# Kernel optimization log

Measured on AMD Instinct MI355X. Metric: run time of the kernel, lower is better.

## Reference

```python
import jax, jax.numpy as jnp
import numpy as np

EPS = 1e-6
N_HEADS, N_POINTS = 6, 4


def layer_norm(x, w, b):
    m = jnp.mean(x, -1, keepdims=True)
    v = jnp.mean((x - m) ** 2, -1, keepdims=True)
    return (x - m) * jax.lax.rsqrt(v + EPS) * w + b


def bilinear_sample(val, loc, Hl, Wl):
    # val: (B, nH, Hl*Wl, d); loc: (B, Lq, nH, P, 2) in [0,1]
    # matches F.grid_sample(mode='bilinear', padding='zeros', align_corners=False)
    B, nH, _, d = val.shape
    Lq, P = loc.shape[1], loc.shape[3]
    x = loc[..., 0] * Wl - 0.5
    y = loc[..., 1] * Hl - 0.5
    x0 = jnp.floor(x)
    y0 = jnp.floor(y)
    wx1 = x - x0
    wy1 = y - y0
    out = jnp.zeros((B, nH, Lq * P, d), val.dtype)
    corners = ((0, 0, (1 - wy1) * (1 - wx1)), (0, 1, (1 - wy1) * wx1),
               (1, 0, wy1 * (1 - wx1)), (1, 1, wy1 * wx1))
    for dy, dx, w in corners:
        xi = x0 + dx
        yi = y0 + dy
        valid = (xi >= 0) & (xi < Wl) & (yi >= 0) & (yi < Hl)
        xi_c = jnp.clip(xi, 0, Wl - 1).astype(jnp.int32)
        yi_c = jnp.clip(yi, 0, Hl - 1).astype(jnp.int32)
        idx = (yi_c * Wl + xi_c).transpose(0, 2, 1, 3).reshape(B, nH, Lq * P)
        g = jnp.take_along_axis(val, idx[..., None], axis=2)  # (B,nH,Lq*P,d)
        ww = jnp.where(valid, w, 0.0).transpose(0, 2, 1, 3).reshape(B, nH, Lq * P)
        out = out + g * ww[..., None]
    return out.reshape(B, nH, Lq, P, d).transpose(0, 2, 1, 3, 4)  # (B,Lq,nH,P,d)


def dwconv3x3(x, w, b):
    # x: (N, C, H, W); w: (C, 1, 3, 3) depthwise
    y = jax.lax.conv_general_dilated(x, w, (1, 1), 'SAME',
                                     feature_group_count=w.shape[0],
                                     dimension_numbers=('NCHW', 'OIHW', 'NCHW'))
    return y + b[None, :, None, None]


def setup_inputs() -> dict:
    key = jax.random.key(0)
    ks = jax.random.split(key, 16)
    B, H, W, C = 8, 32, 32, 768
    Lq = 3 * H * W
    Hf = Wf = 64
    hidden = int(C * 0.25)
    s = 0.02
    inp = {
        'query': jax.random.normal(ks[0], (B, Lq, C), jnp.float32),
        'reference_points': jax.random.uniform(ks[1], (B, Lq, 1, 2), jnp.float32),
        'feat': jax.random.normal(ks[2], (B, Hf * Wf, C), jnp.float32),
        'spatial_shapes': jnp.array([[Hf, Wf]], jnp.int32),
        'level_start_index': jnp.zeros((1,), jnp.int32),
        'H': H, 'W': W,
        'qn_w': jnp.ones((C,)), 'qn_b': jnp.zeros((C,)),
        'fn_w': jnp.ones((C,)), 'fn_b': jnp.zeros((C,)),
        'so_w': jax.random.normal(ks[3], (C, N_HEADS * N_POINTS * 2)) * s,
        'so_b': jax.random.normal(ks[4], (N_HEADS * N_POINTS * 2,)) * s,
        'aw_w': jax.random.normal(ks[5], (C, N_HEADS * N_POINTS)) * s,
        'aw_b': jnp.zeros((N_HEADS * N_POINTS,)),
        'vp_w': jax.random.normal(ks[6], (C, C)) * s,
        'vp_b': jnp.zeros((C,)),
        'op_w': jax.random.normal(ks[7], (C, C)) * s,
        'op_b': jnp.zeros((C,)),
        'ffn_w': jnp.ones((C,)), 'ffn_b': jnp.zeros((C,)),
        'fc1_w': jax.random.normal(ks[8], (C, hidden)) * s,
        'fc1_b': jnp.zeros((hidden,)),
        'dw_w': jax.random.normal(ks[9], (hidden, 1, 3, 3)) * s,
        'dw_b': jnp.zeros((hidden,)),
        'fc2_w': jax.random.normal(ks[10], (hidden, C)) * s,
        'fc2_b': jnp.zeros((C,)),
    }
    return inp


def reference(query, reference_points, feat, spatial_shapes, level_start_index, H, W,
              qn_w, qn_b, fn_w, fn_b, so_w, so_b, aw_w, aw_b, vp_w, vp_b, op_w, op_b,
              ffn_w, ffn_b, fc1_w, fc1_b, dw_w, dw_b, fc2_w, fc2_b):
    B, Lq, C = query.shape
    nH, nP = N_HEADS, N_POINTS
    d = C // nH
    ss = np.asarray(spatial_shapes)
    Hl, Wl = int(ss[0, 0]), int(ss[0, 1])

    # --- MSDeformAttn (single level) ---
    q = layer_norm(query, qn_w, qn_b)
    f = layer_norm(feat, fn_w, fn_b)
    value = (f @ vp_w + vp_b).reshape(B, Hl * Wl, nH, d).transpose(0, 2, 1, 3)  # (B,nH,Lin,d)
    offs = (q @ so_w + so_b).reshape(B, Lq, nH, 1, nP, 2)
    aw = jax.nn.softmax((q @ aw_w + aw_b).reshape(B, Lq, nH, nP), axis=-1)
    normalizer = jnp.array([Wl, Hl], query.dtype)
    loc = reference_points[:, :, None, :, None, :] + offs / normalizer  # (B,Lq,nH,1,nP,2)
    sampled = bilinear_sample(value, loc[:, :, :, 0], Hl, Wl)           # (B,Lq,nH,nP,d)
    attn = (sampled * aw[..., None]).sum(3).reshape(B, Lq, C) @ op_w + op_b
    query = query + attn

    # --- ConvFFN (3 equal HxW chunks through shared depthwise conv) ---
    x = layer_norm(query, ffn_w, ffn_b) @ fc1_w + fc1_b  # (B, 3*H*W, hid)
    n = Lq // 3
    hid = fc1_w.shape[1]
    xc = x.reshape(B, 3, n, hid).transpose(0, 1, 3, 2).reshape(B * 3, hid, H, W)
    xc = dwconv3x3(xc, dw_w, dw_b)
    x = xc.reshape(B, 3, hid, n).transpose(0, 1, 3, 2).reshape(B, Lq, hid)
    x = jax.nn.gelu(x, approximate=False)
    x = x @ fc2_w + fc2_b
    return query + x
```

## Files before the change

### kernel.cpp

```cpp
#include <hip/hip_runtime.h>
#include <hip/hip_bf16.h>
#include <math.h>

typedef __hip_bfloat16 bf16;
typedef short bf16x8 __attribute__((ext_vector_type(8)));
typedef short bf16x4 __attribute__((ext_vector_type(4)));
typedef float f32x4 __attribute__((ext_vector_type(4)));

#define NB 8
#define LQ 3072
#define CC 768
#define NHEADS 6
#define NPTS 4
#define DHEAD 128
#define HLVL 64
#define WLVL 64
#define LIN 4096
#define HID 192
#define BLTOT 24576
#define FROWS 32768

__device__ __forceinline__ float bf2f(short u)
{ return __uint_as_float(((unsigned)(unsigned short)u) << 16); }

template<int N_>
__device__ __forceinline__ void wait_vmcnt()
{
    if constexpr (N_ == 0)      asm volatile("s_waitcnt vmcnt(0)" ::: "memory");
    else if constexpr (N_ == 2) asm volatile("s_waitcnt vmcnt(2)" ::: "memory");
    else if constexpr (N_ == 4) asm volatile("s_waitcnt vmcnt(4)" ::: "memory");
    else if constexpr (N_ == 6) asm volatile("s_waitcnt vmcnt(6)" ::: "memory");
    else if constexpr (N_ == 8) asm volatile("s_waitcnt vmcnt(8)" ::: "memory");
    else static_assert(N_ == 0, "add a vmcnt case");
}

__device__ __forceinline__ void wt_tile(float (*t)[65], const float* __restrict__ src,
                                        bf16* __restrict__ dst, int K, int N, int tn0, int tk0)
{
    const int r = threadIdx.x >> 6, c = threadIdx.x & 63;
    #pragma unroll
    for (int i = 0; i < 16; ++i)
        t[i * 4 + r][c] = src[(size_t)(tk0 + i * 4 + r) * N + tn0 + c];
    __syncthreads();
    #pragma unroll
    for (int i = 0; i < 16; ++i)
        dst[(size_t)(tn0 + i * 4 + r) * K + tk0 + c] = __float2bfloat16(t[c][i * 4 + r]);
}

__global__ __launch_bounds__(256)
void prep_kernel(const float* __restrict__ vp_w, const float* __restrict__ op_w,
                 const float* __restrict__ fc1_w, const float* __restrict__ fc2_w,
                 const float* __restrict__ so_w, const float* __restrict__ so_b,
                 const float* __restrict__ aw_w, const float* __restrict__ aw_b,
                 const float* __restrict__ feat, const float* __restrict__ fn_w,
                 const float* __restrict__ fn_b,
                 bf16* __restrict__ vp_wt, bf16* __restrict__ op_wt,
                 bf16* __restrict__ fc1_wt, bf16* __restrict__ fc2_wt,
                 bf16* __restrict__ dots_wt, float* __restrict__ db,
                 bf16* __restrict__ f_ln)
{
    __shared__ float t[64][65];
    int b = blockIdx.x;
    if (b < 144)      wt_tile(t, vp_w, vp_wt, 768, 768, (b % 12) * 64, (b / 12) * 64);
    else if (b < 288) { b -= 144; wt_tile(t, op_w, op_wt, 768, 768, (b % 12) * 64, (b / 12) * 64); }
    else if (b < 324) { b -= 288; wt_tile(t, fc1_w, fc1_wt, 768, 192, (b % 3) * 64, (b / 3) * 64); }
    else if (b < 360) { b -= 324; wt_tile(t, fc2_w, fc2_wt, 192, 768, (b % 12) * 64, (b / 12) * 64); }
    else if (b < 744) {
        b -= 360;
        int i = b * 256 + threadIdx.x;
        if (i < 128 * 768) {
            int n = i / 768, k = i - n * 768;
            float v = 0.f;
            if (n < 48) v = so_w[(size_t)k * 48 + n];
            else if (n < 72) v = aw_w[(size_t)k * 24 + (n - 48)];
            dots_wt[i] = __float2bfloat16(v);
        }
        if (i < 128) {
            float bv = 0.f;
            if (i < 48) bv = so_b[i];
            else if (i < 72) bv = aw_b[i - 48];
            db[i] = bv;
        }
    } else {
        const int row = (b - 744) * 4 + (threadIdx.x >> 6);
        const int lane = threadIdx.x & 63;
        const f32x4* xr = (const f32x4*)(feat + (size_t)row * CC);
        f32x4 f0 = xr[lane], f1 = xr[64 + lane], f2 = xr[128 + lane];
        float s = 0.f, ss = 0.f;
        #pragma unroll
        for (int k = 0; k < 4; ++k) {
            s += f0[k] + f1[k] + f2[k];
            ss += f0[k] * f0[k] + f1[k] * f1[k] + f2[k] * f2[k];
        }
        #pragma unroll
        for (int o = 32; o > 0; o >>= 1) { s += __shfl_down(s, o); ss += __shfl_down(ss, o); }
        s = __shfl(s, 0); ss = __shfl(ss, 0);
        const float m = s * (1.f / CC);
        const float rs = rsqrtf(ss * (1.f / CC) - m * m + 1e-6f);
        const f32x4* w4 = (const f32x4*)fn_w;
        const f32x4* b4 = (const f32x4*)fn_b;
        bf16* orow = f_ln + (size_t)row * CC;
        #pragma unroll
        for (int j = 0; j < 3; ++j) {
            f32x4 fj = (j == 0) ? f0 : (j == 1) ? f1 : f2;
            f32x4 wj = w4[j * 64 + lane], bj = b4[j * 64 + lane];
            bf16 t4[4];
            #pragma unroll
            for (int k = 0; k < 4; ++k) t4[k] = __float2bfloat16((fj[k] - m) * rs * wj[k] + bj[k]);
            *(bf16x4*)(orow + j * 256 + lane * 4) = *(bf16x4*)t4;
        }
    }
}

template<int BM, int BN, int WM, int WN, int MODE>
__global__ __launch_bounds__(256)
void gemm_kernel(const bf16* __restrict__ A, const bf16* __restrict__ Bt,
                 const float* __restrict__ bias, const void* __restrict__ resv,
                 void* __restrict__ outv, int M, int N, int K)
{
    constexpr int WAVES_N = BN / WN;
    constexpr int FM = WM / 16, FN = WN / 16;
    constexpr int CWA = BM / 32;
    constexpr int CWB = BN / 32;
    constexpr int LPT = CWA + CWB;
    constexpr int ABYTES = BM * 256;
    constexpr int DBUF_BYTES = (BM + BN) * 256;
    constexpr int EPI_BYTES = BM * BN * 4;
    constexpr size_t SMEM_BYTES = DBUF_BYTES > EPI_BYTES ? DBUF_BYTES : EPI_BYTES;
    __shared__ __align__(16) char smem[SMEM_BYTES];
    bf16* sA = (bf16*)smem;
    bf16* sB = (bf16*)(smem + ABYTES);
    float* epi = (float*)smem;

    const int tid = threadIdx.x;
    const int lane = tid & 63;
    const int wave = tid >> 6;

    const int nwgx = gridDim.x;
    const int nwg = nwgx * gridDim.y;
    const int bid = blockIdx.y * nwgx + blockIdx.x;
    const int swz = (bid & 7) * (nwg >> 3) + (bid >> 3);
    const int m0 = (swz / nwgx) * BM;
    const int n0 = (swz % nwgx) * BN;

    const int wm = (wave / WAVES_N) * WM;
    const int wn = (wave % WAVES_N) * WN;

    const int srow = lane >> 3;
    const int scol = ((lane & 7) ^ srow) * 8;

    constexpr int GPR8 = BN / 8;
    constexpr int GPT8 = (BM * BN / 8) / 256;
    constexpr int QPR4 = BN / 4;
    constexpr int QPT4 = (BM * BN / 4) / 256;
    float4 pr0[GPT8], pr1[GPT8];
    bf16x4 prb[QPT4];
    if constexpr (MODE == 3) {
        const float* resf = (const float*)resv;
        #pragma unroll
        for (int k = 0; k < GPT8; ++k) {
            const int f = k * 256 + tid;
            const int rr = f / GPR8, cc = (f % GPR8) * 8;
            const size_t gidx = (size_t)(m0 + rr) * N + n0 + cc;
            pr0[k] = *(const float4*)&resf[gidx];
            pr1[k] = *(const float4*)&resf[gidx + 4];
        }
    }
    if constexpr (MODE == 4) {
        const bf16* resb = (const bf16*)resv;
        #pragma unroll
        for (int k = 0; k < QPT4; ++k) {
            const int f = k * 256 + tid;
            const int rr = f / QPR4, cc = (f % QPR4) * 4;
            prb[k] = *(const bf16x4*)&resb[(size_t)(m0 + rr) * N + n0 + cc];
        }
    }

#define STAGE(tt, half)                                                                            \
    { const int k0_ = (tt) * 64;                                                                   \
      _Pragma("unroll")                                                                            \
      for (int i_ = 0; i_ < CWA; ++i_) {                                                           \
        const int c_ = i_ * 4 + wave;                                                              \
        __builtin_amdgcn_global_load_lds(                                                          \
          (const __attribute__((address_space(1))) void*)(A + (size_t)(m0 + c_ * 8 + srow) * K + k0_ + scol), \
          (__attribute__((address_space(3))) void*)(sA + (half) * (BM * 64) + c_ * 512), 16, 0, 0); } \
      _Pragma("unroll")                                                                            \
      for (int i_ = 0; i_ < CWB; ++i_) {                                                           \
        const int c_ = i_ * 4 + wave;                                                              \
        __builtin_amdgcn_global_load_lds(                                                          \
          (const __attribute__((address_space(1))) void*)(Bt + (size_t)(n0 + c_ * 8 + srow) * K + k0_ + scol), \
          (__attribute__((address_space(3))) void*)(sB + (half) * (BN * 64) + c_ * 512), 16, 0, 0); } }

    f32x4 acc[FM][FN] = {};
    const int nt = K >> 6;

    STAGE(0, 0);
    STAGE(1, 1);

    for (int t = 0; t < nt; ++t) {
        const int half = t & 1;
        if (t + 1 < nt) wait_vmcnt<LPT>();
        else            wait_vmcnt<0>();
        __builtin_amdgcn_s_barrier();
        const bf16* cA = sA + half * (BM * 64);
        const bf16* cB = sB + half * (BN * 64);
        #pragma unroll
        for (int kki = 0; kki < 2; ++kki) {
            const int kslot = kki * 4 + (lane >> 4);
            bf16x8 aF[FM], bF[FN];
            #pragma unroll
            for (int i = 0; i < FM; ++i) {
                const int row = wm + i * 16 + (lane & 15);
                aF[i] = *(const bf16x8*)(&cA[row * 64 + ((kslot ^ (row & 7)) * 8)]);
            }
            #pragma unroll
            for (int j = 0; j < FN; ++j) {
                const int row = wn + j * 16 + (lane & 15);
                bF[j] = *(const bf16x8*)(&cB[row * 64 + ((kslot ^ (row & 7)) * 8)]);
            }
            #pragma unroll
            for (int i = 0; i < FM; ++i) {
                #pragma unroll
                for (int j = 0; j < FN; ++j)
                    acc[i][j] = __builtin_amdgcn_mfma_f32_16x16x32_bf16(aF[i], bF[j], acc[i][j], 0, 0, 0);
            }
        }
        asm volatile("s_waitcnt lgkmcnt(0)" ::: "memory");
        __builtin_amdgcn_s_barrier();
        if (t + 2 < nt) STAGE(t + 2, half);
    }
#undef STAGE

    #pragma unroll
    for (int j = 0; j < FN; ++j) {
        const int colL = wn + j * 16 + (lane & 15);
        const float bj = bias[n0 + colL];
        #pragma unroll
        for (int i = 0; i < FM; ++i) {
            #pragma unroll
            for (int r = 0; r < 4; ++r) {
                const int rowL = wm + i * 16 + ((lane >> 4) << 2) + r;
                const int addr = rowL * BN + ((((colL >> 2) ^ (rowL & 7)) << 2) | (colL & 3));
                epi[addr] = acc[i][j][r] + bj;
            }
        }
    }
    __syncthreads();

    if constexpr (MODE == 0 || MODE == 3) {
        #pragma unroll
        for (int k = 0; k < GPT8; ++k) {
            const int f = k * 256 + tid;
            const int rr = f / GPR8, cc = (f % GPR8) * 8;
            const int g0 = ((cc >> 2) ^ (rr & 7)) << 2;
            const int g1 = (((cc >> 2) + 1) ^ (rr & 7)) << 2;
            float4 v0 = *(const float4*)&epi[rr * BN + g0];
            float4 v1 = *(const float4*)&epi[rr * BN + g1];
            if constexpr (MODE == 3) {
                v0.x += pr0[k].x; v0.y += pr0[k].y; v0.z += pr0[k].z; v0.w += pr0[k].w;
                v1.x += pr1[k].x; v1.y += pr1[k].y; v1.z += pr1[k].z; v1.w += pr1[k].w;
            }
            bf16 tmp[8];
            tmp[0] = __float2bfloat16(v0.x); tmp[1] = __float2bfloat16(v0.y);
            tmp[2] = __float2bfloat16(v0.z); tmp[3] = __float2bfloat16(v0.w);
            tmp[4] = __float2bfloat16(v1.x); tmp[5] = __float2bfloat16(v1.y);
            tmp[6] = __float2bfloat16(v1.z); tmp[7] = __float2bfloat16(v1.w);
            *(bf16x8*)((bf16*)outv + (size_t)(m0 + rr) * N + n0 + cc) = *(bf16x8*)tmp;
        }
    } else {
        #pragma unroll
        for (int k = 0; k < QPT4; ++k) {
            const int f = k * 256 + tid;
            const int rr = f / QPR4, cc = (f % QPR4) * 4;
            const int gs = ((cc >> 2) ^ (rr & 7)) << 2;
            float4 v = *(const float4*)&epi[rr * BN + gs];
            if constexpr (MODE == 4) {
                v.x += bf2f(prb[k][0]); v.y += bf2f(prb[k][1]);
                v.z += bf2f(prb[k][2]); v.w += bf2f(prb[k][3]);
            }
            *(float4*)&((float*)outv)[(size_t)(m0 + rr) * N + n0 + cc] = v;
        }
    }
}

__global__ __launch_bounds__(512)
void gemm_value_kernel(const bf16* __restrict__ A, const bf16* __restrict__ Bt,
                       const float* __restrict__ bias, bf16* __restrict__ outb,
                       int M, int N, int K)
{
    constexpr int BM = 128, BN = 256;
    constexpr int FM = 4, FN = 4;
    constexpr int CWA = 2, CWB = 4;
    constexpr int LPT = CWA + CWB;
    __shared__ __align__(16) char smem[2 * (BM + BN) * 128];
    bf16* sA = (bf16*)smem;
    bf16* sB = (bf16*)(smem + 2 * BM * 128);
    float* epi = (float*)smem;

    const int tid = threadIdx.x;
    const int lane = tid & 63;
    const int wave = tid >> 6;

    const int nwgx = gridDim.x;
    const int nwg = nwgx * gridDim.y;
    const int bid = blockIdx.y * nwgx + blockIdx.x;
    const int swz = (bid & 7) * (nwg >> 3) + (bid >> 3);
    const int m0 = (swz / nwgx) * BM;
    const int n0 = (swz % nwgx) * BN;

    const int wm = (wave >> 2) * 64;
    const int wn = (wave & 3) * 64;
    const int srow = lane >> 3;
    const int scol = ((lane & 7) ^ srow) * 8;

#define STAGEV(tt, half)                                                                           \
    { const int k0_ = (tt) * 64;                                                                   \
      _Pragma("unroll")                                                                            \
      for (int i_ = 0; i_ < CWA; ++i_) {                                                           \
        const int c_ = i_ * 8 + wave;                                                              \
        __builtin_amdgcn_global_load_lds(                                                          \
          (const __attribute__((address_space(1))) void*)(A + (size_t)(m0 + c_ * 8 + srow) * K + k0_ + scol), \
          (__attribute__((address_space(3))) void*)(sA + (half) * (BM * 64) + c_ * 512), 16, 0, 0); } \
      _Pragma("unroll")                                                                            \
      for (int i_ = 0; i_ < CWB; ++i_) {                                                           \
        const int c_ = i_ * 8 + wave;                                                              \
        __builtin_amdgcn_global_load_lds(                                                          \
          (const __attribute__((address_space(1))) void*)(Bt + (size_t)(n0 + c_ * 8 + srow) * K + k0_ + scol), \
          (__attribute__((address_space(3))) void*)(sB + (half) * (BN * 64) + c_ * 512), 16, 0, 0); } }

    f32x4 acc[FM][FN] = {};
    const int nt = K >> 6;

    STAGEV(0, 0);
    STAGEV(1, 1);

    for (int t = 0; t < nt; ++t) {
        const int half = t & 1;
        if (t + 1 < nt) wait_vmcnt<LPT>();
        else            wait_vmcnt<0>();
        __builtin_amdgcn_s_barrier();
        const bf16* cA = sA + half * (BM * 64);
        const bf16* cB = sB + half * (BN * 64);
        #pragma unroll
        for (int kki = 0; kki < 2; ++kki) {
            const int kslot = kki * 4 + (lane >> 4);
            bf16x8 aF[FM], bF[FN];
            #pragma unroll
            for (int i = 0; i < FM; ++i) {
                const int row = wm + i * 16 + (lane & 15);
                aF[i] = *(const bf16x8*)(&cA[row * 64 + ((kslot ^ (row & 7)) * 8)]);
            }
            #pragma unroll
            for (int j = 0; j < FN; ++j) {
                const int row = wn + j * 16 + (lane & 15);
                bF[j] = *(const bf16x8*)(&cB[row * 64 + ((kslot ^ (row & 7)) * 8)]);
            }
            #pragma unroll
            for (int i = 0; i < FM; ++i) {
                #pragma unroll
                for (int j = 0; j < FN; ++j)
                    acc[i][j] = __builtin_amdgcn_mfma_f32_16x16x32_bf16(aF[i], bF[j], acc[i][j], 0, 0, 0);
            }
        }
        asm volatile("s_waitcnt lgkmcnt(0)" ::: "memory");
        __builtin_amdgcn_s_barrier();
        if (t + 2 < nt) STAGEV(t + 2, half);
    }
#undef STAGEV

    for (int half = 0; half < 2; ++half) {
        if ((wave >> 2) == half) {
            #pragma unroll
            for (int j = 0; j < FN; ++j) {
                const int colL = wn + j * 16 + (lane & 15);
                const float bj = bias[n0 + colL];
                #pragma unroll
                for (int i = 0; i < FM; ++i) {
                    #pragma unroll
                    for (int r = 0; r < 4; ++r) {
                        const int lr = i * 16 + ((lane >> 4) << 2) + r;
                        const int addr = lr * BN + ((((colL >> 2) ^ (lr & 7)) << 2) | (colL & 3));
                        epi[addr] = acc[i][j][r] + bj;
                    }
                }
            }
        }
        __syncthreads();
        #pragma unroll
        for (int k = 0; k < 4; ++k) {
            const int f = k * 512 + tid;
            const int rr = f >> 5, cc = (f & 31) * 8;
            const int g0 = ((cc >> 2) ^ (rr & 7)) << 2;
            const int g1 = (((cc >> 2) + 1) ^ (rr & 7)) << 2;
            float4 v0 = *(const float4*)&epi[rr * BN + g0];
            float4 v1 = *(const float4*)&epi[rr * BN + g1];
            bf16 tmp[8];
            tmp[0] = __float2bfloat16(v0.x); tmp[1] = __float2bfloat16(v0.y);
            tmp[2] = __float2bfloat16(v0.z); tmp[3] = __float2bfloat16(v0.w);
            tmp[4] = __float2bfloat16(v1.x); tmp[5] = __float2bfloat16(v1.y);
            tmp[6] = __float2bfloat16(v1.z); tmp[7] = __float2bfloat16(v1.w);
            *(bf16x8*)(outb + (size_t)(m0 + half * 64 + rr) * N + n0 + cc) = *(bf16x8*)tmp;
        }
        __syncthreads();
    }
}

template<int BM, int BN, int WM, int WN, bool F32IN, int EPI>
__global__ __launch_bounds__(256)
void ln_gemm_kernel(const void* __restrict__ xv, const float* __restrict__ lnw,
                    const float* __restrict__ lnb, const bf16* __restrict__ Bt,
                    const float* __restrict__ bias, const float* __restrict__ refp,
                    void* __restrict__ outv, int M, int N)
{
    constexpr int WAVES_N = BN / WN;
    constexpr int FM = WM / 16, FN = WN / 16;
    constexpr int CWB = BN / 32;
    constexpr int RPW = BM / 4;
    static_assert(BM * BN * 4 <= 2 * BN * 64 * 2, "epi must fit in sB");
    __shared__ __align__(16) bf16 sA[BM * 768];
    __shared__ __align__(16) char sBmem[2 * BN * 64 * 2];
    bf16* sB = (bf16*)sBmem;
    float* epi = (float*)sBmem;

    const int tid = threadIdx.x;
    const int lane = tid & 63;
    const int wave = tid >> 6;

    const int nwgx = gridDim.x;
    const int nwg = nwgx * gridDim.y;
    const int bid = blockIdx.y * nwgx + blockIdx.x;
    const int swz = (bid & 7) * (nwg >> 3) + (bid >> 3);
    const int m0 = (swz / nwgx) * BM;
    const int n0 = (swz % nwgx) * BN;

    const int wm = (wave / WAVES_N) * WM;
    const int wn = (wave % WAVES_N) * WN;
    const int srow = lane >> 3;
    const int scol = ((lane & 7) ^ srow) * 8;

#define STAGEB(tt, half)                                                                           \
    { const int k0_ = (tt) * 64;                                                                   \
      _Pragma("unroll")                                                                            \
      for (int i_ = 0; i_ < CWB; ++i_) {                                                           \
        const int c_ = i_ * 4 + wave;                                                              \
        __builtin_amdgcn_global_load_lds(                                                          \
          (const __attribute__((address_space(1))) void*)(Bt + (size_t)(n0 + c_ * 8 + srow) * 768 + k0_ + scol), \
          (__attribute__((address_space(3))) void*)(sB + (half) * (BN * 64) + c_ * 512), 16, 0, 0); } }

    STAGEB(0, 0);
    STAGEB(1, 1);

    if constexpr (F32IN) {
        const f32x4* w4 = (const f32x4*)lnw;
        const f32x4* b4 = (const f32x4*)lnb;
        f32x4 wv0 = w4[lane], wv1 = w4[64 + lane], wv2 = w4[128 + lane];
        f32x4 bv0 = b4[lane], bv1 = b4[64 + lane], bv2 = b4[128 + lane];
        for (int rr = 0; rr < RPW; ++rr) {
            const int r = wave * RPW + rr;
            const f32x4* xr = (const f32x4*)((const float*)xv + (size_t)(m0 + r) * 768);
            f32x4 f0 = xr[lane], f1 = xr[64 + lane], f2 = xr[128 + lane];
            float s = 0.f, ss = 0.f;
            #pragma unroll
            for (int k = 0; k < 4; ++k) {
                s += f0[k] + f1[k] + f2[k];
                ss += f0[k] * f0[k] + f1[k] * f1[k] + f2[k] * f2[k];
            }
            #pragma unroll
            for (int o = 32; o > 0; o >>= 1) { s += __shfl_down(s, o); ss += __shfl_down(ss, o); }
            s = __shfl(s, 0); ss = __shfl(ss, 0);
            const float mn = s * (1.f / 768);
            const float rs = rsqrtf(ss * (1.f / 768) - mn * mn + 1e-6f);
            const int rx7 = r & 7;
            const int slot = (lane >> 1) & 7;
            const int off = (lane & 1) * 4;
            #pragma unroll
            for (int j = 0; j < 3; ++j) {
                f32x4 fj = (j == 0) ? f0 : (j == 1) ? f1 : f2;
                f32x4 wj = (j == 0) ? wv0 : (j == 1) ? wv1 : wv2;
                f32x4 bj = (j == 0) ? bv0 : (j == 1) ? bv1 : bv2;
                bf16 t4[4];
                #pragma unroll
                for (int k = 0; k < 4; ++k)
                    t4[k] = __float2bfloat16((fj[k] - mn) * rs * wj[k] + bj[k]);
                const int kt = j * 4 + (lane >> 4);
                *(bf16x4*)&sA[r * 768 + kt * 64 + ((slot ^ rx7) << 3) + off] = *(bf16x4*)t4;
            }
        }
    } else {
        const f32x4* w4 = (const f32x4*)lnw;
        const f32x4* b4 = (const f32x4*)lnb;
        f32x4 w80 = w4[lane * 2], w81 = w4[lane * 2 + 1], w44 = w4[128 + lane];
        f32x4 b80 = b4[lane * 2], b81 = b4[lane * 2 + 1], b44 = b4[128 + lane];
        for (int rr = 0; rr < RPW; ++rr) {
            const int r = wave * RPW + rr;
            const bf16* xr = (const bf16*)xv + (size_t)(m0 + r) * 768;
            bf16x8 v8 = *(const bf16x8*)(xr + lane * 8);
            bf16x4 v4 = *(const bf16x4*)(xr + 512 + lane * 4);
            float f[12];
            #pragma unroll
            for (int k = 0; k < 8; ++k) f[k] = bf2f(v8[k]);
            #pragma unroll
            for (int k = 0; k < 4; ++k) f[8 + k] = bf2f(v4[k]);
            float s = 0.f, ss = 0.f;
            #pragma unroll
            for (int k = 0; k < 12; ++k) { s += f[k]; ss += f[k] * f[k]; }
            #pragma unroll
            for (int o = 32; o > 0; o >>= 1) { s += __shfl_down(s, o); ss += __shfl_down(ss, o); }
            s = __shfl(s, 0); ss = __shfl(ss, 0);
            const float mn = s * (1.f / 768);
            const float rs = rsqrtf(ss * (1.f / 768) - mn * mn + 1e-6f);
            const int rx7 = r & 7;
            bf16 t8[8];
            #pragma unroll
            for (int k = 0; k < 4; ++k) t8[k] = __float2bfloat16((f[k] - mn) * rs * w80[k] + b80[k]);
            #pragma unroll
            for (int k = 0; k < 4; ++k) t8[4 + k] = __float2bfloat16((f[4 + k] - mn) * rs * w81[k] + b81[k]);
            *(bf16x8*)&sA[r * 768 + (lane >> 3) * 64 + (((lane & 7) ^ rx7) << 3)] = *(bf16x8*)t8;
            bf16 t4[4];
            #pragma unroll
            for (int k = 0; k < 4; ++k) t4[k] = __float2bfloat16((f[8 + k] - mn) * rs * w44[k] + b44[k]);
            *(bf16x4*)&sA[r * 768 + (8 + (lane >> 4)) * 64 + ((((lane >> 1) & 7) ^ rx7) << 3) + (lane & 1) * 4]
                = *(bf16x4*)t4;
        }
    }
    asm volatile("s_waitcnt lgkmcnt(0)" ::: "memory");

    f32x4 acc[FM][FN] = {};
    #pragma unroll
    for (int t = 0; t < 12; ++t) {
        const int half = t & 1;
        if (t + 1 < 12) wait_vmcnt<CWB>();
        else            wait_vmcnt<0>();
        __builtin_amdgcn_s_barrier();
        const bf16* cB = sB + half * (BN * 64);
        #pragma unroll
        for (int kki = 0; kki < 2; ++kki) {
            const int kslot = kki * 4 + (lane >> 4);
            bf16x8 aF[FM], bF[FN];
            #pragma unroll
            for (int i = 0; i < FM; ++i) {
                const int row = wm + i * 16 + (lane & 15);
                aF[i] = *(const bf16x8*)(&sA[row * 768 + t * 64 + ((kslot ^ (row & 7)) * 8)]);
            }
            #pragma unroll
            for (int j = 0; j < FN; ++j) {
                const int row = wn + j * 16 + (lane & 15);
                bF[j] = *(const bf16x8*)(&cB[row * 64 + ((kslot ^ (row & 7)) * 8)]);
            }
            #pragma unroll
            for (int i = 0; i < FM; ++i) {
                #pragma unroll
                for (int j = 0; j < FN; ++j)
                    acc[i][j] = __builtin_amdgcn_mfma_f32_16x16x32_bf16(aF[i], bF[j], acc[i][j], 0, 0, 0);
            }
        }
        asm volatile("s_waitcnt lgkmcnt(0)" ::: "memory");
        __builtin_amdgcn_s_barrier();
        if (t + 2 < 12) STAGEB(t + 2, half);
    }
#undef STAGEB

    #pragma unroll
    for (int j = 0; j < FN; ++j) {
        const int colL = wn + j * 16 + (lane & 15);
        const float bj = bias[n0 + colL];
        #pragma unroll
        for (int i = 0; i < FM; ++i) {
            #pragma unroll
            for (int r = 0; r < 4; ++r) {
                const int rowL = wm + i * 16 + ((lane >> 4) << 2) + r;
                const int addr = rowL * BN + ((((colL >> 2) ^ (rowL & 7)) << 2) | (colL & 3));
                epi[addr] = acc[i][j][r] + bj;
            }
        }
    }
    __syncthreads();

    if constexpr (EPI == 1) {
        if (tid < BM * NHEADS) {
            const int rowL = tid & (BM - 1);
            const int h = tid / BM;
            auto erd = [&](int col) -> float {
                return epi[rowL * BN + ((((col >> 2) ^ (rowL & 7)) << 2) | (col & 3))];
            };
            float l0 = erd(48 + h * 4 + 0), l1 = erd(48 + h * 4 + 1);
            float l2 = erd(48 + h * 4 + 2), l3 = erd(48 + h * 4 + 3);
            float mx = fmaxf(fmaxf(l0, l1), fmaxf(l2, l3));
            float e0 = expf(l0 - mx), e1 = expf(l1 - mx), e2 = expf(l2 - mx), e3 = expf(l3 - mx);
            float inv = 1.f / (e0 + e1 + e2 + e3);
            float ee[4] = {e0, e1, e2, e3};
            const float rx = refp[(size_t)(m0 + rowL) * 2];
            const float ry = refp[(size_t)(m0 + rowL) * 2 + 1];
            float4* pp = (float4*)outv + ((size_t)(m0 + rowL) * NHEADS + h) * 4;
            #pragma unroll
            for (int p = 0; p < 4; ++p) {
                float ox = erd(h * 8 + p * 2), oy = erd(h * 8 + p * 2 + 1);
                pp[p] = make_float4(rx + ox * (1.f / WLVL), ry + oy * (1.f / HLVL), ee[p] * inv, 0.f);
            }
        }
    } else {
        constexpr int GPR8 = BN / 8;
        constexpr int GPT8 = (BM * BN / 8) / 256;
        #pragma unroll
        for (int k = 0; k < GPT8; ++k) {
            const int f = k * 256 + tid;
            const int rr = f / GPR8, cc = (f % GPR8) * 8;
            const int g0 = ((cc >> 2) ^ (rr & 7)) << 2;
            const int g1 = (((cc >> 2) + 1) ^ (rr & 7)) << 2;
            float4 v0 = *(const float4*)&epi[rr * BN + g0];
            float4 v1 = *(const float4*)&epi[rr * BN + g1];
            bf16 tmp[8];
            tmp[0] = __float2bfloat16(v0.x); tmp[1] = __float2bfloat16(v0.y);
            tmp[2] = __float2bfloat16(v0.z); tmp[3] = __float2bfloat16(v0.w);
            tmp[4] = __float2bfloat16(v1.x); tmp[5] = __float2bfloat16(v1.y);
            tmp[6] = __float2bfloat16(v1.z); tmp[7] = __float2bfloat16(v1.w);
            *(bf16x8*)((bf16*)outv + (size_t)(m0 + rr) * N + n0 + cc) = *(bf16x8*)tmp;
        }
    }
}

__global__ __launch_bounds__(256)
void sampler_kernel(const bf16* __restrict__ value, const float4* __restrict__ params,
                    bf16* __restrict__ attn_in)
{
    const int tid = threadIdx.x;
    const int cpx = gridDim.x >> 3;
    const int gblk = (blockIdx.x & 7) * cpx + (blockIdx.x >> 3);
    const int g = gblk * 16 + (tid >> 4);
    const int lane16 = tid & 15;
    const int bl = g / NHEADS;
    const int h = g - bl * NHEADS;
    const int b = bl / LQ;
    const bf16* vh = value + (size_t)b * LIN * CC + h * DHEAD + lane16 * 8;

    int offs[16];
    float wgt[16];
    #pragma unroll
    for (int p = 0; p < NPTS; ++p) {
        float4 pr = params[(size_t)g * 4 + p];
        float x = pr.x * (float)WLVL - 0.5f;
        float y = pr.y * (float)HLVL - 0.5f;
        float x0f = floorf(x), y0f = floorf(y);
        float wx1 = x - x0f, wy1 = y - y0f;
        float wx0 = 1.f - wx1, wy0 = 1.f - wy1;
        int x0 = (int)x0f, y0 = (int)y0f;
        #pragma unroll
        for (int dy = 0; dy < 2; ++dy) {
            const int yi = y0 + dy;
            const int yc = min(max(yi, 0), HLVL - 1);
            const float wy = (dy ? wy1 : wy0) * ((yi >= 0 && yi < HLVL) ? pr.z : 0.f);
            #pragma unroll
            for (int dx = 0; dx < 2; ++dx) {
                const int xi = x0 + dx;
                const int xc = min(max(xi, 0), WLVL - 1);
                const int idx = p * 4 + dy * 2 + dx;
                offs[idx] = (yc * WLVL + xc) * CC;
                wgt[idx] = wy * (dx ? wx1 : wx0) * ((xi >= 0 && xi < WLVL) ? 1.f : 0.f);
            }
        }
    }
    bf16x8 v[16];
    #pragma unroll
    for (int i = 0; i < 16; ++i) v[i] = *(const bf16x8*)(vh + offs[i]);
    float acc[8] = {};
    #pragma unroll
    for (int i = 0; i < 16; ++i) {
        #pragma unroll
        for (int j = 0; j < 8; ++j)
            acc[j] += wgt[i] * bf2f(v[i][j]);
    }
    bf16 tmp[8];
    #pragma unroll
    for (int j = 0; j < 8; ++j) tmp[j] = __float2bfloat16(acc[j]);
    *(bf16x8*)(attn_in + (size_t)bl * CC + h * DHEAD + lane16 * 8) = *(bf16x8*)tmp;
}

__global__ __launch_bounds__(192)
void dwconv_gelu_kernel(const bf16* __restrict__ z, const float* __restrict__ dw_w,
                        const float* __restrict__ dw_b, bf16* __restrict__ g)
{
    const int tp = threadIdx.x / 48;
    const int tc = threadIdx.x % 48;
    const int m = blockIdx.x * 4 + tp;
    const int c = tc * 4;
    const int pix = m & 1023;
    const int h = pix >> 5, w = pix & 31;
    float acc[4];
    #pragma unroll
    for (int j = 0; j < 4; ++j) acc[j] = dw_b[c + j];
    #pragma unroll
    for (int dy = -1; dy <= 1; ++dy) {
        int hh2 = h + dy;
        if (hh2 < 0 || hh2 >= 32) continue;
        #pragma unroll
        for (int dx = -1; dx <= 1; ++dx) {
            int ww2 = w + dx;
            if (ww2 < 0 || ww2 >= 32) continue;
            bf16x4 vv = *(const bf16x4*)&z[(size_t)(m + dy * 32 + dx) * HID + c];
            #pragma unroll
            for (int j = 0; j < 4; ++j)
                acc[j] += bf2f(vv[j]) * dw_w[(c + j) * 9 + (dy + 1) * 3 + (dx + 1)];
        }
    }
    bf16 tmp[4];
    #pragma unroll
    for (int j = 0; j < 4; ++j) {
        float ge = acc[j] * 0.5f * (1.f + erff(acc[j] * 0.70710678118f));
        tmp[j] = __float2bfloat16(ge);
    }
    *(bf16x4*)&g[(size_t)m * HID + c] = *(bf16x4*)tmp;
}

extern "C" void kernel_launch(void* const* d_in, const int* in_sizes, int n_in,
                              void* d_out, int out_size, void* d_ws, size_t ws_size,
                              hipStream_t stream)
{
    const float* query = (const float*)d_in[0];
    const float* refp  = (const float*)d_in[1];
    const float* feat  = (const float*)d_in[2];
    const float* qn_w = (const float*)d_in[7];
    const float* qn_b = (const float*)d_in[8];
    const float* fn_w = (const float*)d_in[9];
    const float* fn_b = (const float*)d_in[10];
    const float* so_w = (const float*)d_in[11];
    const float* so_b = (const float*)d_in[12];
    const float* aw_w = (const float*)d_in[13];
    const float* aw_b = (const float*)d_in[14];
    const float* vp_w = (const float*)d_in[15];
    const float* vp_b = (const float*)d_in[16];
    const float* op_w = (const float*)d_in[17];
    const float* op_b = (const float*)d_in[18];
    const float* ffn_w = (const float*)d_in[19];
    const float* ffn_b = (const float*)d_in[20];
    const float* fc1_w = (const float*)d_in[21];
    const float* fc1_b = (const float*)d_in[22];
    const float* dw_w = (const float*)d_in[23];
    const float* dw_b = (const float*)d_in[24];
    const float* fc2_w = (const float*)d_in[25];
    const float* fc2_b = (const float*)d_in[26];
    float* out = (float*)d_out;

    if (ws_size < (size_t)125829632) return;
    char* ws = (char*)d_ws;
    bf16* vp_wt   = (bf16*)(ws + 0);
    bf16* op_wt   = (bf16*)(ws + 1179648);
    bf16* fc1_wt  = (bf16*)(ws + 2359296);
    bf16* fc2_wt  = (bf16*)(ws + 2654208);
    bf16* dots_wt = (bf16*)(ws + 2949120);
    float* dots_b = (float*)(ws + 3145728);
    char* paramsR = ws + 3146240;
    char* dotsR   = ws + 12583424;
    char* regA = ws + 25166336;
    char* regB = ws + 75497984;
    float4* params = (float4*)paramsR;
    bf16* g        = (bf16*)paramsR;
    bf16* z        = (bf16*)dotsR;
    bf16* f_ln    = (bf16*)regA;
    bf16* attn_in = (bf16*)regA;
    bf16* value = (bf16*)regB;
    bf16* s_bf  = (bf16*)regB;

    prep_kernel<<<744 + FROWS / 4, 256, 0, stream>>>(
        vp_w, op_w, fc1_w, fc2_w, so_w, so_b, aw_w, aw_b, feat, fn_w, fn_b,
        vp_wt, op_wt, fc1_wt, fc2_wt, dots_wt, dots_b, f_ln);

    ln_gemm_kernel<32, 128, 16, 64, true, 1><<<dim3(1, BLTOT / 32), 256, 0, stream>>>(
        query, qn_w, qn_b, dots_wt, dots_b, refp, params, BLTOT, 128);
    gemm_value_kernel<<<dim3(3, FROWS / 128), 512, 0, stream>>>(
        f_ln, vp_wt, vp_b, value, FROWS, 768, 768);
    sampler_kernel<<<(BLTOT * NHEADS) / 16, 256, 0, stream>>>(value, params, attn_in);
    gemm_kernel<64, 128, 32, 64, 3><<<dim3(6, BLTOT / 64), 256, 0, stream>>>(
        attn_in, op_wt, op_b, query, s_bf, BLTOT, 768, 768);

    ln_gemm_kernel<32, 64, 32, 16, false, 0><<<dim3(3, BLTOT / 32), 256, 0, stream>>>(
        s_bf, ffn_w, ffn_b, fc1_wt, fc1_b, nullptr, z, BLTOT, HID);
    dwconv_gelu_kernel<<<BLTOT / 4, 192, 0, stream>>>(z, dw_w, dw_b, g);
    gemm_kernel<64, 128, 32, 64, 4><<<dim3(6, BLTOT / 64), 256, 0, stream>>>(
        g, fc2_wt, fc2_b, s_bf, out, BLTOT, 768, HID);
}
```

Baseline: 308.1 us.

## Shrink value GEMM tile to 128x128 and reorder sampler blocks by head

```diff
diff --git a/kernel.cpp b/kernel.cpp
--- a/kernel.cpp
+++ b/kernel.cpp
@@ -288,10 +288,9 @@
                        const float* __restrict__ bias, bf16* __restrict__ outb,
                        int M, int N, int K)
 {
-    constexpr int BM = 128, BN = 256;
-    constexpr int FM = 4, FN = 4;
-    constexpr int CWA = 2, CWB = 4;
-    constexpr int LPT = CWA + CWB;
+    constexpr int BM = 128, BN = 128;
+    constexpr int FM = 2, FN = 4;
+    constexpr int LPT = 4;
     __shared__ __align__(16) char smem[2 * (BM + BN) * 128];
     bf16* sA = (bf16*)smem;
     bf16* sB = (bf16*)(smem + 2 * BM * 128);
@@ -308,21 +307,21 @@
     const int m0 = (swz / nwgx) * BM;
     const int n0 = (swz % nwgx) * BN;
 
-    const int wm = (wave >> 2) * 64;
-    const int wn = (wave & 3) * 64;
+    const int wm = (wave >> 1) * 32;
+    const int wn = (wave & 1) * 64;
     const int srow = lane >> 3;
     const int scol = ((lane & 7) ^ srow) * 8;
 
 #define STAGEV(tt, half)                                                                           \
     { const int k0_ = (tt) * 64;                                                                   \
       _Pragma("unroll")                                                                            \
-      for (int i_ = 0; i_ < CWA; ++i_) {                                                           \
+      for (int i_ = 0; i_ < 2; ++i_) {                                                             \
         const int c_ = i_ * 8 + wave;                                                              \
         __builtin_amdgcn_global_load_lds(                                                          \
           (const __attribute__((address_space(1))) void*)(A + (size_t)(m0 + c_ * 8 + srow) * K + k0_ + scol), \
           (__attribute__((address_space(3))) void*)(sA + (half) * (BM * 64) + c_ * 512), 16, 0, 0); } \
       _Pragma("unroll")                                                                            \
-      for (int i_ = 0; i_ < CWB; ++i_) {                                                           \
+      for (int i_ = 0; i_ < 2; ++i_) {                                                             \
         const int c_ = i_ * 8 + wave;                                                              \
         __builtin_amdgcn_global_load_lds(                                                          \
           (const __attribute__((address_space(1))) void*)(Bt + (size_t)(n0 + c_ * 8 + srow) * K + k0_ + scol), \
@@ -368,40 +367,35 @@
     }
 #undef STAGEV
 
-    for (int half = 0; half < 2; ++half) {
-        if ((wave >> 2) == half) {
-            #pragma unroll
-            for (int j = 0; j < FN; ++j) {
-                const int colL = wn + j * 16 + (lane & 15);
-                const float bj = bias[n0 + colL];
-                #pragma unroll
-                for (int i = 0; i < FM; ++i) {
-                    #pragma unroll
-                    for (int r = 0; r < 4; ++r) {
-                        const int lr = i * 16 + ((lane >> 4) << 2) + r;
-                        const int addr = lr * BN + ((((colL >> 2) ^ (lr & 7)) << 2) | (colL & 3));
-                        epi[addr] = acc[i][j][r] + bj;
-                    }
-                }
-            }
-        }
-        __syncthreads();
-        #pragma unroll
-        for (int k = 0; k < 4; ++k) {
-            const int f = k * 512 + tid;
-            const int rr = f >> 5, cc = (f & 31) * 8;
-            const int g0 = ((cc >> 2) ^ (rr & 7)) << 2;
-            const int g1 = (((cc >> 2) + 1) ^ (rr & 7)) << 2;
-            float4 v0 = *(const float4*)&epi[rr * BN + g0];
-            float4 v1 = *(const float4*)&epi[rr * BN + g1];
-            bf16 tmp[8];
-            tmp[0] = __float2bfloat16(v0.x); tmp[1] = __float2bfloat16(v0.y);
-            tmp[2] = __float2bfloat16(v0.z); tmp[3] = __float2bfloat16(v0.w);
-            tmp[4] = __float2bfloat16(v1.x); tmp[5] = __float2bfloat16(v1.y);
-            tmp[6] = __float2bfloat16(v1.z); tmp[7] = __float2bfloat16(v1.w);
-            *(bf16x8*)(outb + (size_t)(m0 + half * 64 + rr) * N + n0 + cc) = *(bf16x8*)tmp;
-        }
-        __syncthreads();
+    #pragma unroll
+    for (int j = 0; j < FN; ++j) {
+        const int colL = wn + j * 16 + (lane & 15);
+        const float bj = bias[n0 + colL];
+        #pragma unroll
+        for (int i = 0; i < FM; ++i) {
+            #pragma unroll
+            for (int r = 0; r < 4; ++r) {
+                const int rowL = wm + i * 16 + ((lane >> 4) << 2) + r;
+                const int addr = rowL * BN + ((((colL >> 2) ^ (rowL & 7)) << 2) | (colL & 3));
+                epi[addr] = acc[i][j][r] + bj;
+            }
+        }
+    }
+    __syncthreads();
+    #pragma unroll
+    for (int k = 0; k < 4; ++k) {
+        const int f = k * 512 + tid;
+        const int rr = f >> 4, cc = (f & 15) * 8;
+        const int g0 = ((cc >> 2) ^ (rr & 7)) << 2;
+        const int g1 = (((cc >> 2) + 1) ^ (rr & 7)) << 2;
+        float4 v0 = *(const float4*)&epi[rr * BN + g0];
+        float4 v1 = *(const float4*)&epi[rr * BN + g1];
+        bf16 tmp[8];
+        tmp[0] = __float2bfloat16(v0.x); tmp[1] = __float2bfloat16(v0.y);
+        tmp[2] = __float2bfloat16(v0.z); tmp[3] = __float2bfloat16(v0.w);
+        tmp[4] = __float2bfloat16(v1.x); tmp[5] = __float2bfloat16(v1.y);
+        tmp[6] = __float2bfloat16(v1.z); tmp[7] = __float2bfloat16(v1.w);
+        *(bf16x8*)(outb + (size_t)(m0 + rr) * N + n0 + cc) = *(bf16x8*)tmp;
     }
 }
 
@@ -624,13 +618,13 @@
                     bf16* __restrict__ attn_in)
 {
     const int tid = threadIdx.x;
-    const int cpx = gridDim.x >> 3;
-    const int gblk = (blockIdx.x & 7) * cpx + (blockIdx.x >> 3);
-    const int g = gblk * 16 + (tid >> 4);
+    const int b = blockIdx.x & 7;
+    const int local = blockIdx.x >> 3;
+    const int h = local / 192;
+    const int qc = local - h * 192;
+    const int bl = b * LQ + qc * 16 + (tid >> 4);
+    const int g = bl * NHEADS + h;
     const int lane16 = tid & 15;
-    const int bl = g / NHEADS;
-    const int h = g - bl * NHEADS;
-    const int b = bl / LQ;
     const bf16* vh = value + (size_t)b * LIN * CC + h * DHEAD + lane16 * 8;
 
     int offs[16];
@@ -766,7 +760,7 @@
 
     ln_gemm_kernel<32, 128, 16, 64, true, 1><<<dim3(1, BLTOT / 32), 256, 0, stream>>>(
         query, qn_w, qn_b, dots_wt, dots_b, refp, params, BLTOT, 128);
-    gemm_value_kernel<<<dim3(3, FROWS / 128), 512, 0, stream>>>(
+    gemm_value_kernel<<<dim3(6, FROWS / 128), 512, 0, stream>>>(
         f_ln, vp_wt, vp_b, value, FROWS, 768, 768);
     sampler_kernel<<<(BLTOT * NHEADS) / 16, 256, 0, stream>>>(value, params, attn_in);
     gemm_kernel<64, 128, 32, 64, 3><<<dim3(6, BLTOT / 64), 256, 0, stream>>>(
```

Measured after the change: 301.1 us. 2.3% less time.
